# Kernel tuning notes

Hardware: AMD Instinct MI355X
Metric: run time of the kernel (lower is better)

Reference implementation:

```python
import jax, jax.numpy as jnp
import numpy as np

N_E = 1024
E_DIM = 64
BETA = 0.25
DECAY = 0.99
EPSILON = 1e-5


def setup_inputs() -> dict:
    key = jax.random.key(0)
    k1, k2, k3 = jax.random.split(key, 3)
    z = jax.random.normal(k1, (32, E_DIM, 32, 32), dtype=jnp.float32)
    # codebook initialized uniform(-1/n_e, 1/n_e) as in the torch module
    emb_w = jax.random.uniform(k2, (N_E, E_DIM), minval=-1.0 / N_E, maxval=1.0 / N_E, dtype=jnp.float32)
    ema_cluster_size = jnp.ones((N_E,), dtype=jnp.float32)
    ema_w = jax.random.uniform(k3, (N_E, E_DIM), minval=-1.0 / N_E, maxval=1.0 / N_E, dtype=jnp.float32)
    return {"z": z, "emb_w": emb_w, "ema_cluster_size": ema_cluster_size, "ema_w": ema_w}


def reference(z, emb_w, ema_cluster_size, ema_w):
    B, C, H, W = z.shape  # C == E_DIM
    zf = jnp.transpose(z, (0, 2, 3, 1)).reshape(-1, E_DIM)  # [N, e_dim]
    N = zf.shape[0]

    # squared-distance via ||z||^2 + ||e||^2 - 2 z.e (same expansion as torch code)
    d = (jnp.sum(zf * zf, axis=1, keepdims=True)
         + jnp.sum(emb_w * emb_w, axis=1)
         - 2.0 * zf @ emb_w.T)  # [N, n_e]
    idx = jnp.argmin(d, axis=1)  # [N]

    min_encodings = jax.nn.one_hot(idx, N_E, dtype=jnp.float32)  # [N, n_e]
    # cluster stats via scatter-add (equivalent to one-hot matmuls, cheaper)
    cluster_size = jax.ops.segment_sum(jnp.ones((N,), jnp.float32), idx, num_segments=N_E)
    sum_encodings = jax.ops.segment_sum(zf, idx, num_segments=N_E)  # [n_e, e_dim]

    # EMA update (training path, done before the z_q lookup as in torch)
    new_cs = DECAY * ema_cluster_size + (1.0 - DECAY) * cluster_size
    new_w = DECAY * ema_w + (1.0 - DECAY) * sum_encodings
    n = jnp.sum(new_cs)
    cs_norm = (new_cs + EPSILON) / (n + N_E * EPSILON) * n
    new_emb = new_w / cs_norm[:, None]  # updated codebook

    z_q = new_emb[idx].reshape(B, H, W, C).transpose(0, 3, 1, 2)  # [B,C,H,W]
    loss = BETA * jnp.mean((jax.lax.stop_gradient(z_q) - z) ** 2)
    z_q_st = z + jax.lax.stop_gradient(z_q - z)  # straight-through

    avg_probs = cluster_size / N
    perplexity = jnp.exp(-jnp.sum(avg_probs * jnp.log(avg_probs + 1e-10)))
    return loss, z_q_st, perplexity, min_encodings, idx
```

## Files before the change

### kernel.cpp

```cpp
#include <hip/hip_runtime.h>
#include <math.h>

#define NVEC 32768
#define NE   1024
#define ED   64
#define TOT  2097152
#define NCHUNK 4
#define CHUNK  128
#define MT     128

#define O_LOSS   0
#define O_ZQ     1
#define O_PERP   2097153
#define O_MINENC 2097154
#define O_IDX    35651586

#define W_PIDX   0
#define W_CS     32768
#define W_SUMENC 33792
#define W_ESQ    164864


__global__ void __launch_bounds__(256) k_pre(const float* __restrict__ emb,
                                             float* __restrict__ ws,
                                             float* __restrict__ out) {
    int b = blockIdx.x;
    if (b < 65) {
        int i = b * 256 + threadIdx.x;
        float4 zv; zv.x = 0.f; zv.y = 0.f; zv.z = 0.f; zv.w = 0.f;
        *(float4*)(ws + W_CS + i * 4) = zv;
        if (b == 0 && threadIdx.x == 0) out[O_LOSS] = 0.f;
    } else {
        int code = (b - 65) * 256 + threadIdx.x;
        const float* ep = emb + (size_t)code * ED;
        float r[8];
#pragma unroll
        for (int j = 0; j < 8; ++j) r[j] = __fmul_rn(ep[j], ep[j]);
#pragma unroll
        for (int i = 8; i < 64; i += 8)
#pragma unroll
            for (int j = 0; j < 8; ++j)
                r[j] = __fadd_rn(r[j], __fmul_rn(ep[i + j], ep[i + j]));
        ws[W_ESQ + code] = __fadd_rn(
            __fadd_rn(__fadd_rn(r[0], r[1]), __fadd_rn(r[2], r[3])),
            __fadd_rn(__fadd_rn(r[4], r[5]), __fadd_rn(r[6], r[7])));
    }
}

__device__ __forceinline__ int apos(int m) {
    return ((m & 4) << 4) + ((m >> 3) << 2) + (m & 3);
}

__global__ void __launch_bounds__(256) k_dist(const float* __restrict__ z,
                                              const float* __restrict__ emb,
                                              const float* __restrict__ esq_g,
                                              float* __restrict__ out) {
    __shared__ __align__(16) float s_a[64 * 128];
    __shared__ __align__(16) float s_b[64 * 132];
    __shared__ float s_esq[CHUNK];
    __shared__ float s_zsq[MT];

    int tid = threadIdx.x;
    int tile = blockIdx.x >> 1, khalf = blockIdx.x & 1;
    int n0 = tile * MT;
    int b = n0 >> 10, hw0 = n0 & 1023;
    const float* zb = z + b * 65536 + hw0;

#pragma unroll
    for (int j = 0; j < 8; ++j) {
        int f4i = j * 256 + tid;
        int q = f4i & 31, c = f4i >> 5;
        float4 v = *(const float4*)(zb + (c << 10) + q * 4);
        v.x = __fmul_rn(2.0f, v.x);
        v.y = __fmul_rn(2.0f, v.y);
        v.z = __fmul_rn(2.0f, v.z);
        v.w = __fmul_rn(2.0f, v.w);
        *(float4*)(s_a + c * 128 + ((q & 1) << 6) + ((q >> 1) << 2)) = v;
    }
    __syncthreads();

    if (tid < MT) {
        int p = apos(tid);
        float r[8];
#pragma unroll
        for (int j = 0; j < 8; ++j) {
            float v = s_a[j * 128 + p];
            r[j] = __fmul_rn(v, v);
        }
#pragma unroll
        for (int i = 8; i < 64; i += 8)
#pragma unroll
            for (int j = 0; j < 8; ++j) {
                float v = s_a[(i + j) * 128 + p];
                r[j] = __fadd_rn(r[j], __fmul_rn(v, v));
            }
        s_zsq[tid] = __fmul_rn(0.25f, __fadd_rn(
            __fadd_rn(__fadd_rn(r[0], r[1]), __fadd_rn(r[2], r[3])),
            __fadd_rn(__fadd_rn(r[4], r[5]), __fadd_rn(r[6], r[7]))));
    }
    __syncthreads();

    int mi = tid & 15, ki = tid >> 4;
    int kbase = ki * 8;
    float zs[8];
#pragma unroll
    for (int mu = 0; mu < 8; ++mu) zs[mu] = s_zsq[8 * mi + mu];

    float bd[8];
    int bix[8];
#pragma unroll
    for (int mu = 0; mu < 8; ++mu) { bd[mu] = 3.4e38f; bix[mu] = khalf * 512 + kbase; }

    for (int ch = 0; ch < NCHUNK; ++ch) {
        int k0 = khalf * 512 + ch * CHUNK;
        __syncthreads();
#pragma unroll
        for (int j = 0; j < 8; ++j) {
            int f4i = j * 256 + tid;
            int kl = f4i >> 4, c4 = f4i & 15;
            float4 v = *(const float4*)(emb + (size_t)(k0 + kl) * ED + c4 * 4);
            int base = (((kl >> 2) + c4) & 31) * 4 + (kl & 3);
            s_b[(c4 * 4 + 0) * 132 + base] = v.x;
            s_b[(c4 * 4 + 1) * 132 + base] = v.y;
            s_b[(c4 * 4 + 2) * 132 + base] = v.z;
            s_b[(c4 * 4 + 3) * 132 + base] = v.w;
        }
        if (tid < CHUNK) s_esq[tid] = esq_g[k0 + tid];
        __syncthreads();

        float acc[8][8];
#pragma unroll
        for (int mu = 0; mu < 8; ++mu)
#pragma unroll
            for (int ku = 0; ku < 8; ++ku) acc[mu][ku] = 0.f;

        for (int cg = 0; cg < 64; cg += 4) {
            float4 A0[4], A1[4], B0[4], B1[4];
#pragma unroll
            for (int j = 0; j < 4; ++j) {
                int c = cg + j;
                int c4 = c >> 2;
                const float* ar = s_a + c * 128 + (mi << 2);
                A0[j] = *(const float4*)(ar);
                A1[j] = *(const float4*)(ar + 64);
                B0[j] = *(const float4*)(s_b + c * 132 + ((2 * ki + c4) & 31) * 4);
                B1[j] = *(const float4*)(s_b + c * 132 + ((2 * ki + 1 + c4) & 31) * 4);
            }
#pragma unroll
            for (int j = 0; j < 4; ++j) {
#pragma unroll
                for (int mu = 0; mu < 8; ++mu) {
                    float a = (mu < 4) ? (&A0[j].x)[mu] : (&A1[j].x)[mu - 4];
                    acc[mu][0] = __fmaf_rn(a, B0[j].x, acc[mu][0]);
                    acc[mu][1] = __fmaf_rn(a, B0[j].y, acc[mu][1]);
                    acc[mu][2] = __fmaf_rn(a, B0[j].z, acc[mu][2]);
                    acc[mu][3] = __fmaf_rn(a, B0[j].w, acc[mu][3]);
                    acc[mu][4] = __fmaf_rn(a, B1[j].x, acc[mu][4]);
                    acc[mu][5] = __fmaf_rn(a, B1[j].y, acc[mu][5]);
                    acc[mu][6] = __fmaf_rn(a, B1[j].z, acc[mu][6]);
                    acc[mu][7] = __fmaf_rn(a, B1[j].w, acc[mu][7]);
                }
            }
        }

#pragma unroll
        for (int mu = 0; mu < 8; ++mu)
#pragma unroll
            for (int ku = 0; ku < 8; ++ku) {
                float d = __fsub_rn(__fadd_rn(zs[mu], s_esq[kbase + ku]),
                                    acc[mu][ku]);
                if (d < bd[mu]) { bd[mu] = d; bix[mu] = k0 + kbase + ku; }
            }
    }

    __syncthreads();
    float* red_d = s_b;
    int* red_i = (int*)(s_b + 2048);
#pragma unroll
    for (int mu = 0; mu < 8; ++mu) {
        red_d[ki * 128 + 8 * mi + mu] = bd[mu];
        red_i[ki * 128 + 8 * mi + mu] = bix[mu];
    }
    __syncthreads();
    if (tid < MT) {
        float best = red_d[tid];
        int bi = red_i[tid];
#pragma unroll
        for (int q = 1; q < 16; ++q) {
            float d = red_d[q * 128 + tid];
            int i = red_i[q * 128 + tid];
            if (d < best || (d == best && i < bi)) { best = d; bi = i; }
        }
        out[O_MINENC + khalf * 32768 + n0 + tid] = best;
        ((int*)(out + O_MINENC))[65536 + khalf * 32768 + n0 + tid] = bi;
    }
}

__global__ void __launch_bounds__(256) k_mrg(const float* __restrict__ z,
                                             int* __restrict__ fidx,
                                             int* __restrict__ cnt,
                                             float* __restrict__ sumenc,
                                             float* __restrict__ out) {
    __shared__ int s_bi[MT];
    int tid = threadIdx.x;
    int m0 = blockIdx.x * MT;

    if (tid < MT) {
        int m = m0 + tid;
        const float* cd = out + O_MINENC;
        const int* ci = (const int*)(out + O_MINENC) + 65536;
        float d0 = cd[m], d1 = cd[32768 + m];
        int i0 = ci[m], i1 = ci[32768 + m];
        int bi = (d1 < d0) ? i1 : i0;
        fidx[m] = bi;
        out[O_IDX + m] = (float)bi;
        s_bi[tid] = bi;
        atomicAdd(&cnt[bi], 1);
    }
    __syncthreads();

    int lane = tid & 63, w = tid >> 6;
    int b = m0 >> 10, hw0 = m0 & 1023;
    const float* zc = z + b * 65536 + lane * 1024 + hw0;
#pragma unroll
    for (int t0 = 0; t0 < 32; t0 += 4) {
        float v[4];
#pragma unroll
        for (int u = 0; u < 4; ++u) {
            int ml = (w << 5) + t0 + u;
            v[u] = zc[ml];
        }
#pragma unroll
        for (int u = 0; u < 4; ++u) {
            int ml = (w << 5) + t0 + u;
            unsafeAtomicAdd(sumenc + ((size_t)s_bi[ml] << 6) + lane, v[u]);
        }
    }
}

__global__ void __launch_bounds__(256) k_zq(const float* __restrict__ z,
                                            const int* __restrict__ idx,
                                            const float* __restrict__ ema_cs,
                                            const float* __restrict__ ema_w,
                                            const int* __restrict__ cnt,
                                            const float* __restrict__ sumenc,
                                            float* __restrict__ out) {
    __shared__ float s_csn[NE];
    __shared__ float swn[4], swe[4];
    __shared__ int sbi[16];
    int tid = threadIdx.x;
    bool doent = (blockIdx.x == 0);

    float myncs[4];
    float rn = 0.f, re = 0.f;
#pragma unroll
    for (int j = 0; j < 4; ++j) {
        int k = j * 256 + tid;
        float c = (float)cnt[k];
        float ncs = 0.99f * ema_cs[k] + (1.0f - 0.99f) * c;
        myncs[j] = ncs;
        rn += ncs;
        if (doent) {
            float p = c * (1.0f / (float)NVEC);
            re += p * logf(p + 1e-10f);
        }
    }
#pragma unroll
    for (int o = 32; o > 0; o >>= 1) {
        rn += __shfl_down(rn, o, 64);
        re += __shfl_down(re, o, 64);
    }
    int wave = tid >> 6;
    if ((tid & 63) == 0) { swn[wave] = rn; swe[wave] = re; }
    if (tid < 16) sbi[tid] = idx[blockIdx.x * 16 + tid];
    __syncthreads();
    float nt = (swn[0] + swn[1]) + (swn[2] + swn[3]);
    if (doent && tid == 0) {
        float te = (swe[0] + swe[1]) + (swe[2] + swe[3]);
        out[O_PERP] = expf(-te);
    }
#pragma unroll
    for (int j = 0; j < 4; ++j) {
        int k = j * 256 + tid;
        s_csn[k] = (myncs[j] + 1e-5f) / (nt + 1024.0f * 1e-5f) * nt;
    }
    __syncthreads();

    float local = 0.f;
#pragma unroll
    for (int i = 0; i < 4; ++i) {
        int t = blockIdx.x * 256 + tid + i * 524288;
        int b = t >> 16, c = (t >> 10) & 63, hw = t & 1023;
        int n = (b << 10) | hw;
        int g = idx[n] * ED + c;
        float nw = 0.99f * ema_w[g] + (1.0f - 0.99f) * sumenc[g];
        float e = nw / s_csn[g >> 6];
        float zv = z[t];
        float diff = e - zv;
        out[O_ZQ + t] = zv + diff;
        local = fmaf(diff, diff, local);
    }

    int t = tid;
    int r0 = blockIdx.x * 16;
    for (int r = 0; r < 16; ++r) {
        int rbi = sbi[r];
        float* rp = out + O_MINENC + (size_t)(r0 + r) * NE;
        if (t < 254) {
            int col = 2 + t * 4;
            float4 v;
            v.x = (col == rbi) ? 1.0f : 0.0f;
            v.y = (col + 1 == rbi) ? 1.0f : 0.0f;
            v.z = (col + 2 == rbi) ? 1.0f : 0.0f;
            v.w = (col + 3 == rbi) ? 1.0f : 0.0f;
            *(float4*)(rp + col) = v;
        } else if (t == 254) {
            float2 v;
            v.x = (0 == rbi) ? 1.0f : 0.0f;
            v.y = (1 == rbi) ? 1.0f : 0.0f;
            *(float2*)(rp) = v;
        } else {
            float4 v;
            v.x = (1018 == rbi) ? 1.0f : 0.0f;
            v.y = (1019 == rbi) ? 1.0f : 0.0f;
            v.z = (1020 == rbi) ? 1.0f : 0.0f;
            v.w = (1021 == rbi) ? 1.0f : 0.0f;
            *(float4*)(rp + 1018) = v;
            float2 w;
            w.x = (1022 == rbi) ? 1.0f : 0.0f;
            w.y = (1023 == rbi) ? 1.0f : 0.0f;
            *(float2*)(rp + 1022) = w;
        }
    }

#pragma unroll
    for (int o = 32; o > 0; o >>= 1) local += __shfl_down(local, o, 64);
    __shared__ float sp[4];
    if ((tid & 63) == 0) sp[wave] = local;
    __syncthreads();
    if (tid == 0)
        unsafeAtomicAdd(out + O_LOSS,
                        ((sp[0] + sp[1]) + (sp[2] + sp[3])) * (0.25f / (float)TOT));
}

extern "C" void kernel_launch(void* const* d_in, const int* in_sizes, int n_in,
                              void* d_out, int out_size, void* d_ws, size_t ws_size,
                              hipStream_t stream) {
    const float* z      = (const float*)d_in[0];
    const float* emb    = (const float*)d_in[1];
    const float* ema_cs = (const float*)d_in[2];
    const float* ema_w  = (const float*)d_in[3];
    float* out = (float*)d_out;
    float* ws  = (float*)d_ws;

    k_pre<<<69, 256, 0, stream>>>(emb, ws, out);
    k_dist<<<512, 256, 0, stream>>>(z, emb, ws + W_ESQ, out);
    k_mrg<<<256, 256, 0, stream>>>(z, (int*)(ws + W_PIDX), (int*)(ws + W_CS),
                                   ws + W_SUMENC, out);
    k_zq<<<2048, 256, 0, stream>>>(z, (const int*)(ws + W_PIDX), ema_cs, ema_w,
                                   (const int*)(ws + W_CS), ws + W_SUMENC, out);
}
```

Before: 246.0 us.

## Fuse argmin merge and scatter-add into distance kernel via per-tile ticket

Removes the separate merge kernel. Each distance block records its partial argmin, then takes a per-tile ticket. The second block of each tile pair merges both halves, writes the final index, bumps the cluster counts and scatter-adds z into the per-code sums, reusing the z tile already held in shared memory instead of re-reading global memory. This saves one kernel launch and a global re-read of z, at the cost of threadfence/ticket synchronisation and extra tail work in half the blocks. The ticket array is zeroed by extending the pre-kernel's clearing range.

```diff
diff --git a/kernel.cpp b/kernel.cpp
--- a/kernel.cpp
+++ b/kernel.cpp
@@ -18,6 +18,7 @@
 #define W_PIDX   0
 #define W_CS     32768
 #define W_SUMENC 33792
+#define W_TICKET 99328
 #define W_ESQ    164864
 
 
@@ -25,13 +26,13 @@
                                              float* __restrict__ ws,
                                              float* __restrict__ out) {
     int b = blockIdx.x;
-    if (b < 65) {
+    if (b < 66) {
         int i = b * 256 + threadIdx.x;
         float4 zv; zv.x = 0.f; zv.y = 0.f; zv.z = 0.f; zv.w = 0.f;
         *(float4*)(ws + W_CS + i * 4) = zv;
         if (b == 0 && threadIdx.x == 0) out[O_LOSS] = 0.f;
     } else {
-        int code = (b - 65) * 256 + threadIdx.x;
+        int code = (b - 66) * 256 + threadIdx.x;
         const float* ep = emb + (size_t)code * ED;
         float r[8];
 #pragma unroll
@@ -54,11 +55,18 @@
 __global__ void __launch_bounds__(256) k_dist(const float* __restrict__ z,
                                               const float* __restrict__ emb,
                                               const float* __restrict__ esq_g,
+                                              int* __restrict__ fidx,
+                                              int* __restrict__ cnt,
+                                              float* __restrict__ sumenc,
+                                              int* __restrict__ ticket,
                                               float* __restrict__ out) {
     __shared__ __align__(16) float s_a[64 * 128];
     __shared__ __align__(16) float s_b[64 * 132];
     __shared__ float s_esq[CHUNK];
     __shared__ float s_zsq[MT];
+    __shared__ float s_bd[MT];
+    __shared__ int s_bi[MT];
+    __shared__ int s_tk;
 
     int tid = threadIdx.x;
     int tile = blockIdx.x >> 1, khalf = blockIdx.x & 1;
@@ -193,47 +201,53 @@
         }
         out[O_MINENC + khalf * 32768 + n0 + tid] = best;
         ((int*)(out + O_MINENC))[65536 + khalf * 32768 + n0 + tid] = bi;
-    }
-}
-
-__global__ void __launch_bounds__(256) k_mrg(const float* __restrict__ z,
-                                             int* __restrict__ fidx,
-                                             int* __restrict__ cnt,
-                                             float* __restrict__ sumenc,
-                                             float* __restrict__ out) {
-    __shared__ int s_bi[MT];
-    int tid = threadIdx.x;
-    int m0 = blockIdx.x * MT;
-
-    if (tid < MT) {
-        int m = m0 + tid;
-        const float* cd = out + O_MINENC;
-        const int* ci = (const int*)(out + O_MINENC) + 65536;
-        float d0 = cd[m], d1 = cd[32768 + m];
-        int i0 = ci[m], i1 = ci[32768 + m];
-        int bi = (d1 < d0) ? i1 : i0;
-        fidx[m] = bi;
-        out[O_IDX + m] = (float)bi;
+        s_bd[tid] = best;
         s_bi[tid] = bi;
-        atomicAdd(&cnt[bi], 1);
-    }
-    __syncthreads();
-
-    int lane = tid & 63, w = tid >> 6;
-    int b = m0 >> 10, hw0 = m0 & 1023;
-    const float* zc = z + b * 65536 + lane * 1024 + hw0;
-#pragma unroll
-    for (int t0 = 0; t0 < 32; t0 += 4) {
-        float v[4];
-#pragma unroll
-        for (int u = 0; u < 4; ++u) {
-            int ml = (w << 5) + t0 + u;
-            v[u] = zc[ml];
-        }
-#pragma unroll
-        for (int u = 0; u < 4; ++u) {
-            int ml = (w << 5) + t0 + u;
-            unsafeAtomicAdd(sumenc + ((size_t)s_bi[ml] << 6) + lane, v[u]);
+    }
+    __threadfence();
+    __syncthreads();
+    if (tid == 0) s_tk = atomicAdd(ticket + tile, 1);
+    __syncthreads();
+    if (s_tk == 0) return;
+    __threadfence();
+
+    {
+        const volatile float* vd = out + O_MINENC;
+        const volatile int* vi = ((const int*)(out + O_MINENC)) + 65536;
+        int oh = khalf ^ 1;
+        if (tid < MT) {
+            float od = vd[oh * 32768 + n0 + tid];
+            int oi = vi[oh * 32768 + n0 + tid];
+            float md = s_bd[tid];
+            int mi_ = s_bi[tid];
+            int bi2 = (od < md || (od == md && oi < mi_)) ? oi : mi_;
+            fidx[n0 + tid] = bi2;
+            out[O_IDX + n0 + tid] = (float)bi2;
+            s_bi[tid] = bi2;
+            atomicAdd(&cnt[bi2], 1);
+        }
+    }
+    __syncthreads();
+
+    {
+        int m = tid & 127, qt = tid >> 7;
+        int p = apos(m);
+#pragma unroll
+        for (int j = 0; j < 32; ++j) {
+            int c = qt * 32 + j;
+            s_b[m * 65 + c] = __fmul_rn(0.5f, s_a[c * 128 + p]);
+        }
+    }
+    __syncthreads();
+
+    {
+        int lane = tid & 63, w = tid >> 6;
+#pragma unroll
+        for (int t = 0; t < 32; ++t) {
+            int m = (w << 5) | t;
+            int bi = s_bi[m];
+            float v = s_b[m * 65 + lane];
+            unsafeAtomicAdd(sumenc + ((size_t)bi << 6) + lane, v);
         }
     }
 }
@@ -353,10 +367,10 @@
     float* out = (float*)d_out;
     float* ws  = (float*)d_ws;
 
-    k_pre<<<69, 256, 0, stream>>>(emb, ws, out);
-    k_dist<<<512, 256, 0, stream>>>(z, emb, ws + W_ESQ, out);
-    k_mrg<<<256, 256, 0, stream>>>(z, (int*)(ws + W_PIDX), (int*)(ws + W_CS),
-                                   ws + W_SUMENC, out);
+    k_pre<<<70, 256, 0, stream>>>(emb, ws, out);
+    k_dist<<<512, 256, 0, stream>>>(z, emb, ws + W_ESQ, (int*)(ws + W_PIDX),
+                                    (int*)(ws + W_CS), ws + W_SUMENC,
+                                    (int*)(ws + W_TICKET), out);
     k_zq<<<2048, 256, 0, stream>>>(z, (const int*)(ws + W_PIDX), ema_cs, ema_w,
                                    (const int*)(ws + W_CS), ws + W_SUMENC, out);
 }
```

New measurement: 273.4 us. +11.1%, slower.
